# Optimization experiments

Hardware: AMD Instinct MI355X
Metric: run time of the kernel (lower is better)

## Reference

```python
import math
import jax, jax.numpy as jnp
import numpy as np

# Gemma4Audio config constants
HID = 1024
H = 8
D = HID // H            # 128
CHUNK = 12              # attention_chunk_size
PAST = 13 - 1           # max_past_horizon = context_left - 1
FUT = 0                 # max_future_horizon = context_right
CTX = CHUNK + PAST + FUT  # 24
SOFTCAP = 50.0
Q_SCALE = D ** (-0.5) / math.log(2)
K_SCALE = math.log(1.0 + math.e) / math.log(2)


def setup_inputs() -> dict:
    key = jax.random.key(0)
    ks = jax.random.split(key, 8)
    B, S = 4, 6144
    P = CTX + 1  # 25 relative positions
    std = HID ** (-0.5)
    return {
        "hidden_states": jax.random.normal(ks[0], (B, S, HID), jnp.float32),
        "position_embeddings": jax.random.normal(ks[1], (P, HID), jnp.float32),
        "Wq": jax.random.normal(ks[2], (HID, HID), jnp.float32) * std,
        "Wk": jax.random.normal(ks[3], (HID, HID), jnp.float32) * std,
        "Wv": jax.random.normal(ks[4], (HID, HID), jnp.float32) * std,
        "Wpost": jax.random.normal(ks[5], (HID, HID), jnp.float32) * std,
        "Wrel": jax.random.normal(ks[6], (HID, HID), jnp.float32) * std,
        "per_dim_scale": jnp.zeros((D,), jnp.float32),  # torch init: zeros
    }


def _extract_block_context(x, num_blocks):
    # x: [B, S, H, D] -> [B, num_blocks, CTX, H, D]
    xp = jnp.pad(x, ((0, 0), (PAST, FUT + CHUNK - 1), (0, 0), (0, 0)))
    idx = jnp.arange(num_blocks)[:, None] * CHUNK + jnp.arange(CTX)[None, :]
    return xp[:, idx]  # gather along seq axis


def _rel_shift(x):
    # x: [B, H, nb, CHUNK, P] -> [B, H, nb, CHUNK, CTX]
    B, Hh, nb, bs, pos_len = x.shape
    x = jnp.pad(x, ((0, 0), (0, 0), (0, 0), (0, 0), (0, CTX + 1 - pos_len)))
    x = x.reshape(B, Hh, nb, bs * (CTX + 1))[..., : bs * CTX]
    return x.reshape(B, Hh, nb, bs, CTX)


def reference(hidden_states, position_embeddings, Wq, Wk, Wv, Wpost, Wrel, per_dim_scale):
    B, S, _ = hidden_states.shape
    nb = (S + CHUNK - 1) // CHUNK
    pad = nb * CHUNK - S

    # Projections (ClippableLinear clamps are +/-inf at init -> identity)
    q = (hidden_states @ Wq.T).reshape(B, S, H, D)
    k = (hidden_states @ Wk.T).reshape(B, S, H, D)
    v = (hidden_states @ Wv.T).reshape(B, S, H, D)

    q = q * (Q_SCALE * jax.nn.softplus(per_dim_scale))  # per-dim scaled queries
    k = k * K_SCALE

    # [B, nb, CHUNK, H, D]
    q_blocked = jnp.pad(q, ((0, 0), (0, pad), (0, 0), (0, 0))).reshape(B, nb, CHUNK, H, D)
    k_ctx = _extract_block_context(k, nb)  # [B, nb, CTX, H, D]
    v_ctx = _extract_block_context(v, nb)

    # content score: [B, H, nb, CHUNK, CTX]
    matrix_ac = jnp.einsum('bnchd,bnkhd->bhnck', q_blocked, k_ctx)

    # relative position score
    rel_k = (position_embeddings @ Wrel.T).reshape(-1, H, D)  # [P, H, D]
    matrix_bd = jnp.einsum('bnchd,phd->bhncp', q_blocked, rel_k)
    matrix_bd = _rel_shift(matrix_bd)  # [B, H, nb, CHUNK, CTX]

    logits = matrix_ac + matrix_bd
    logits = jnp.tanh(logits / SOFTCAP) * SOFTCAP  # softcap
    attn = jax.nn.softmax(logits, axis=-1)

    out = jnp.einsum('bhnck,bnkhd->bnchd', attn, v_ctx)
    out = out.reshape(B, nb * CHUNK, H * D)[:, :S]
    return out @ Wpost.T
```

## Files before the change

kernel.cpp:

```cpp
#include <hip/hip_runtime.h>
#include <hip/hip_bf16.h>
#include <math.h>

typedef unsigned short ushort_t;
typedef __attribute__((ext_vector_type(8))) short short8;
typedef __attribute__((ext_vector_type(4))) short s4v;
typedef __attribute__((ext_vector_type(4))) float float4v;

#define HID 1024
#define NH 8
#define DH 128
#define CHUNK 12
#define PAST 12
#define CTX 24
#define NPOS 25
#define QKVW 3072

__device__ __forceinline__ float bf2f(ushort_t b){
  union{unsigned int u; float f;} x; x.u = ((unsigned int)b)<<16; return x.f;
}
__device__ __forceinline__ ushort_t f2bf(float f){
  union{float f; unsigned int u;} x; x.f = f;
  unsigned int u = x.u;
  unsigned int r = u + 0x7fffu + ((u>>16)&1u);
  return (ushort_t)(r>>16);
}

__device__ __forceinline__ void gload16(const ushort_t* g, ushort_t* l){
  __builtin_amdgcn_global_load_lds(
      (const __attribute__((address_space(1))) unsigned int*)g,
      (__attribute__((address_space(3))) unsigned int*)l,
      16, 0, 0);
}

__global__ __launch_bounds__(256) void cvt_f2b(
    const float* __restrict__ in, ushort_t* __restrict__ out, int n4)
{
  for (int i = blockIdx.x*256 + threadIdx.x; i < n4; i += gridDim.x*256){
    float4v v = ((const float4v*)in)[i];
    s4v o;
#pragma unroll
    for (int j=0;j<4;j++) o[j] = (short)f2bf(v[j]);
    ((s4v*)out)[i] = o;
  }
}

__global__ __launch_bounds__(256) void cvt_w4(
    const float* __restrict__ Wq, const float* __restrict__ Wk,
    const float* __restrict__ Wv, const float* __restrict__ Wp,
    ushort_t* __restrict__ Wcat, ushort_t* __restrict__ Wpb, int wsz4)
{
  for (int i = blockIdx.x*256 + threadIdx.x; i < 4*wsz4; i += gridDim.x*256){
    int seg = i / wsz4, off = i - seg*wsz4;
    const float* src = (seg==0) ? Wq : (seg==1) ? Wk : (seg==2) ? Wv : Wp;
    float4v v = ((const float4v*)src)[off];
    s4v o;
#pragma unroll
    for (int j=0;j<4;j++) o[j] = (short)f2bf(v[j]);
    if (seg < 3) ((s4v*)Wcat)[seg*wsz4 + off] = o;
    else         ((s4v*)Wpb)[off] = o;
  }
}

template<int MODE, int OUTF>
__global__ __launch_bounds__(512) void gemm8(
    const ushort_t* __restrict__ A, const ushort_t* __restrict__ W,
    void* __restrict__ Cv, int M, int N, int K,
    const float* __restrict__ pds, float qsc, float ksc)
{
  const int nwg  = gridDim.x;
  const int orig = blockIdx.x;
  const int qch  = nwg >> 3, rch = nwg & 7;
  const int xcd  = orig & 7, idx = orig >> 3;
  const int bid  = (xcd < rch ? xcd*(qch+1) : rch*(qch+1) + (xcd-rch)*qch) + idx;

  const int NT = N >> 8;
  const int m0 = (bid / NT) * 256;
  const int n0 = (bid % NT) * 256;

  const int tid  = threadIdx.x;
  const int w    = tid >> 6, lane = tid & 63;
  const int wm   = w >> 2, wn = w & 3;
  const int lr   = lane & 15;
  const int lg   = lane >> 4;

  __shared__ ushort_t lds[2][2][256*64];

  float4v acc[2][4][4];
#pragma unroll
  for (int mh=0; mh<2; mh++)
#pragma unroll
    for (int i=0;i<4;i++)
#pragma unroll
      for (int j=0;j<4;j++) acc[mh][i][j] = (float4v)0.0f;

  const int srow = lane >> 3;
  const int sg   = ((lane & 7) ^ srow) * 8;

  const ushort_t* Ab = A + (size_t)m0 * K;
  const ushort_t* Wb = W + (size_t)n0 * K;

#define STAGE_C(c, buf, kt) do {                                              \
    const int rr_ = (c)*64 + w*8 + srow;                                      \
    gload16(Ab + (size_t)rr_*K + (kt) + sg, &lds[buf][0][((c)*64 + w*8)*64]); \
    gload16(Wb + (size_t)rr_*K + (kt) + sg, &lds[buf][1][((c)*64 + w*8)*64]); \
  } while(0)

  short8 bfr[4];

#define PHASE(buf, mh, kh, LOADB) do {                                        \
    short8 afr[4];                                                            \
    _Pragma("unroll")                                                         \
    for (int i=0;i<4;i++){                                                    \
      const int r_ = wm*128 + (mh)*64 + i*16 + lr;                            \
      const int s_ = (((kh)>>3) + lg) ^ (r_ & 7);                             \
      afr[i] = *(const short8*)&lds[buf][0][r_*64 + s_*8];                    \
    }                                                                         \
    if (LOADB){                                                               \
      _Pragma("unroll")                                                       \
      for (int j=0;j<4;j++){                                                  \
        const int r_ = wn*64 + j*16 + lr;                                     \
        const int s_ = (((kh)>>3) + lg) ^ (r_ & 7);                           \
        bfr[j] = *(const short8*)&lds[buf][1][r_*64 + s_*8];                  \
      }                                                                       \
    }                                                                         \
    __builtin_amdgcn_s_setprio(1);                                            \
    _Pragma("unroll")                                                         \
    for (int i=0;i<4;i++)                                                     \
      _Pragma("unroll")                                                       \
      for (int j=0;j<4;j++)                                                   \
        acc[mh][i][j] = __builtin_amdgcn_mfma_f32_16x16x32_bf16(              \
            afr[i], bfr[j], acc[mh][i][j], 0,0,0);                            \
    __builtin_amdgcn_s_setprio(0);                                            \
    __builtin_amdgcn_s_barrier();                                             \
  } while(0)

  const int NTiles = K >> 6;
  STAGE_C(0, 0, 0); STAGE_C(1, 0, 0); STAGE_C(2, 0, 0); STAGE_C(3, 0, 0);
  __syncthreads();

  for (int t = 0; t < NTiles; ++t){
    const int cur = t & 1, nxt = cur ^ 1;
    const int ktn = (t+1) << 6;
    const bool pf = (t+1 < NTiles);
    if (pf) STAGE_C(0, nxt, ktn);
    PHASE(cur, 0, 0, 1);
    if (pf) STAGE_C(1, nxt, ktn);
    PHASE(cur, 1, 0, 0);
    if (pf) STAGE_C(2, nxt, ktn);
    PHASE(cur, 0, 32, 1);
    if (pf) STAGE_C(3, nxt, ktn);
    PHASE(cur, 1, 32, 0);
    __syncthreads();
  }
#undef STAGE_C
#undef PHASE

#pragma unroll
  for (int j=0;j<4;j++){
    const int col = n0 + wn*64 + j*16 + lr;
    float scale = 1.0f;
    if (MODE==1){
      if (col < 1024){ float p = pds[col & (DH-1)]; scale = qsc * log1pf(expf(p)); }
      else if (col < 2048) scale = ksc;
    }
#pragma unroll
    for (int mh=0; mh<2; mh++)
#pragma unroll
      for (int i=0;i<4;i++){
        const int row = m0 + wm*128 + mh*64 + i*16 + lg*4;
#pragma unroll
        for (int r=0;r<4;r++){
          float val = acc[mh][i][j][r] * scale;
          if (OUTF) ((float*)Cv)[(size_t)(row + r)*N + col] = val;
          else ((ushort_t*)Cv)[(size_t)(row + r)*N + col] = f2bf(val);
        }
      }
  }
}

template<int MODE, int OUTF>
__global__ __launch_bounds__(256) void gemm2(
    const ushort_t* __restrict__ A, const ushort_t* __restrict__ W,
    void* __restrict__ Cv, int M, int N, int K,
    const float* __restrict__ pds, float qsc, float ksc)
{
  const int nwg  = gridDim.x;
  const int orig = blockIdx.x;
  const int qch  = nwg >> 3, rch = nwg & 7;
  const int xcd  = orig & 7, idx = orig >> 3;
  const int bid  = (xcd < rch ? xcd*(qch+1) : rch*(qch+1) + (xcd-rch)*qch) + idx;

  const int NT = N >> 7;
  const int m0 = (bid / NT) * 128;
  const int n0 = (bid % NT) * 128;

  const int tid  = threadIdx.x;
  const int w    = tid >> 6, lane = tid & 63;
  const int wm   = w >> 1, wn = w & 1;
  const int lr   = lane & 15;
  const int lg   = lane >> 4;

  __shared__ ushort_t As0[128*32], Bs0[128*32];
  __shared__ ushort_t As1[128*32], Bs1[128*32];

  float4v acc[4][4];
#pragma unroll
  for (int i=0;i<4;i++)
#pragma unroll
    for (int j=0;j<4;j++) acc[i][j] = (float4v)0.0f;

  const int sr = lane >> 2;
  const int sc = (lane & 3) * 8;

  const ushort_t* Ab0 = A + (size_t)(m0 + w*16      + sr)*K + sc;
  const ushort_t* Ab1 = A + (size_t)(m0 + 64 + w*16 + sr)*K + sc;
  const ushort_t* Bb0 = W + (size_t)(n0 + w*16      + sr)*K + sc;
  const ushort_t* Bb1 = W + (size_t)(n0 + 64 + w*16 + sr)*K + sc;

#define STAGE(Abuf, Bbuf, kt) do {                    \
    gload16(Ab0 + (kt), &(Abuf)[(w*16)*32]);          \
    gload16(Ab1 + (kt), &(Abuf)[(64 + w*16)*32]);     \
    gload16(Bb0 + (kt), &(Bbuf)[(w*16)*32]);          \
    gload16(Bb1 + (kt), &(Bbuf)[(64 + w*16)*32]);     \
  } while(0)

#define COMPUTE(Abuf, Bbuf) do {                                             \
    short8 afr[4], bfr[4];                                                   \
    _Pragma("unroll")                                                        \
    for (int i=0;i<4;i++) afr[i] = *(const short8*)&(Abuf)[(wm*64 + i*16 + lr)*32 + lg*8]; \
    _Pragma("unroll")                                                        \
    for (int j=0;j<4;j++) bfr[j] = *(const short8*)&(Bbuf)[(wn*64 + j*16 + lr)*32 + lg*8]; \
    _Pragma("unroll")                                                        \
    for (int i=0;i<4;i++)                                                    \
      _Pragma("unroll")                                                      \
      for (int j=0;j<4;j++)                                                  \
        acc[i][j] = __builtin_amdgcn_mfma_f32_16x16x32_bf16(afr[i], bfr[j], acc[i][j], 0,0,0); \
  } while(0)

  const int nt = K >> 5;
  STAGE(As0, Bs0, 0);
  __syncthreads();

  for (int t = 0; t < nt; t += 2){
    if (t+1 < nt) STAGE(As1, Bs1, (t+1)*32);
    COMPUTE(As0, Bs0);
    __syncthreads();
    if (t+2 < nt) STAGE(As0, Bs0, (t+2)*32);
    COMPUTE(As1, Bs1);
    __syncthreads();
  }
#undef STAGE
#undef COMPUTE

#pragma unroll
  for (int j=0;j<4;j++){
    int col = n0 + wn*64 + j*16 + lr;
    float scale = 1.0f;
    if (MODE==1){
      if (col < 1024){ float p = pds[col & (DH-1)]; scale = qsc * log1pf(expf(p)); }
      else if (col < 2048) scale = ksc;
    }
#pragma unroll
    for (int i=0;i<4;i++){
      int row = m0 + wm*64 + i*16 + lg*4;
#pragma unroll
      for (int r=0;r<4;r++){
        float val = acc[i][j][r] * scale;
        if (OUTF) ((float*)Cv)[(size_t)(row + r)*N + col] = val;
        else ((ushort_t*)Cv)[(size_t)(row + r)*N + col] = f2bf(val);
      }
    }
  }
}

__global__ __launch_bounds__(256) void relk_kernel(
    const float* __restrict__ pe, const float* __restrict__ Wrel,
    ushort_t* __restrict__ rel)
{
  int gid = blockIdx.x*256 + threadIdx.x;
  if (gid >= NPOS*HID) return;
  int p = gid >> 10, n = gid & 1023;
  const float* a = pe + p*HID;
  const float* w = Wrel + (size_t)n*HID;
  float s = 0.f;
  for (int k=0;k<HID;k+=4){
    float4v av = *(const float4v*)(a+k);
    float4v wv = *(const float4v*)(w+k);
#pragma unroll
    for (int u=0;u<4;u++) s += av[u]*wv[u];
  }
  rel[gid] = f2bf(s);
}

__global__ __launch_bounds__(256) void attn_kernel(
  const ushort_t* __restrict__ qkv, const ushort_t* __restrict__ rel,
  ushort_t* __restrict__ o, int S)
{
  const int n0 = blockIdx.x * 4;
  const int b  = blockIdx.y, h = blockIdx.z;
  const int tid = threadIdx.x;
  const size_t bS = (size_t)b * S;

  __shared__ ushort_t ks[68][136];
  __shared__ ushort_t vt[128][68];
  __shared__ ushort_t rs[32][136];
  __shared__ float    sA[4][12][36];
  __shared__ float    sB[4][12][36];
  __shared__ ushort_t Pp[4][16][40];

  const int base = n0*CHUNK - PAST;
  {
    const int r0 = tid >> 4;
    const int c0 = (tid & 15) * 8;
    for (int r = r0; r < 68; r += 16){
      int s = base + r;
      short8 kv = (short8)0, vv = (short8)0;
      if (r < 60 && s >= 0 && s < S){
        kv = *(const short8*)&qkv[(bS + s)*QKVW + 1024 + h*DH + c0];
        vv = *(const short8*)&qkv[(bS + s)*QKVW + 2048 + h*DH + c0];
      }
      *(short8*)&ks[r][c0] = kv;
#pragma unroll
      for (int u=0;u<8;u++) vt[c0+u][r] = (ushort_t)vv[u];
    }
    for (int r = r0; r < 32; r += 16){
      short8 rv = (short8)0;
      if (r < NPOS) rv = *(const short8*)&rel[r*HID + h*DH + c0];
      *(short8*)&rs[r][c0] = rv;
    }
  }
  __syncthreads();

  const int w    = tid >> 6;
  const int lane = tid & 63;
  const int lr   = lane & 15;
  const int lg   = lane >> 4;

  int qrow = (n0 + w)*CHUNK + lr;
  if (qrow >= S) qrow = S - 1;
  const ushort_t* qp = qkv + (bS + qrow)*QKVW + h*DH + lg*8;
  short8 qf[4];
#pragma unroll
  for (int ks2=0; ks2<4; ks2++) qf[ks2] = *(const short8*)(qp + ks2*32);

#pragma unroll
  for (int t0=0; t0<2; t0++){
    float4v acc = (float4v)0.0f;
#pragma unroll
    for (int ks2=0; ks2<4; ks2++){
      short8 kf = *(const short8*)&ks[w*CHUNK + t0*16 + lr][ks2*32 + lg*8];
      acc = __builtin_amdgcn_mfma_f32_16x16x32_bf16(qf[ks2], kf, acc, 0,0,0);
    }
#pragma unroll
    for (int reg=0; reg<4; reg++){
      int cr = lg*4 + reg;
      if (cr < CHUNK) sA[w][cr][t0*16 + lr] = acc[reg];
    }
  }

#pragma unroll
  for (int t0=0; t0<2; t0++){
    float4v acc = (float4v)0.0f;
#pragma unroll
    for (int ks2=0; ks2<4; ks2++){
      short8 rf = *(const short8*)&rs[t0*16 + lr][ks2*32 + lg*8];
      acc = __builtin_amdgcn_mfma_f32_16x16x32_bf16(qf[ks2], rf, acc, 0,0,0);
    }
#pragma unroll
    for (int reg=0; reg<4; reg++){
      int cr = lg*4 + reg;
      if (cr < CHUNK) sB[w][cr][t0*16 + lr] = acc[reg];
    }
  }

#pragma unroll
  for (int i=0;i<2;i++){
    int idx = i*64 + lane;
    *(s4v*)&Pp[w][idx>>3][(idx&7)*4] = (s4v)0;
  }

  {
    const int c2 = lane >> 5;
    const int t  = lane & 31;
#pragma unroll
    for (int i=0;i<6;i++){
      int c = i*2 + c2;
      float x = -1e30f;
      if (t < CTX){
        int f = c*CTX + t;
        int r = f / NPOS, p = f - r*NPOS;
        x = sA[w][c][t] + sB[w][r][p];
        x = 50.0f * tanhf(x * 0.02f);
      }
      float m = x;
      for (int off=16; off>=1; off>>=1) m = fmaxf(m, __shfl_xor(m, off, 32));
      float e = (t < CTX) ? expf(x - m) : 0.0f;
      float s = e;
      for (int off=16; off>=1; off>>=1) s += __shfl_xor(s, off, 32);
      if (t < CTX) Pp[w][c][t] = f2bf(e / s);
    }
  }

  short8 pf = *(const short8*)&Pp[w][lr][lg*8];
  const int orow_base = (n0 + w)*CHUNK;
#pragma unroll
  for (int j=0; j<8; j++){
    int d  = j*16 + lr;
    int tb = w*CHUNK + lg*8;
    s4v b0 = *(const s4v*)&vt[d][tb];
    s4v b1 = *(const s4v*)&vt[d][tb+4];
    short8 bf;
#pragma unroll
    for (int u=0;u<4;u++){ bf[u] = b0[u]; bf[u+4] = b1[u]; }
    float4v a = __builtin_amdgcn_mfma_f32_16x16x32_bf16(pf, bf, (float4v)0.0f, 0,0,0);
#pragma unroll
    for (int reg=0; reg<4; reg++){
      int cr = lg*4 + reg;
      if (cr < CHUNK)
        o[(bS + orow_base + cr)*HID + h*DH + j*16 + lr] = f2bf(a[reg]);
    }
  }
}

extern "C" void kernel_launch(void* const* d_in, const int* in_sizes, int n_in,
                              void* d_out, int out_size, void* d_ws, size_t ws_size,
                              hipStream_t stream)
{
  const float* hs    = (const float*)d_in[0];
  const float* pe    = (const float*)d_in[1];
  const float* Wq    = (const float*)d_in[2];
  const float* Wk    = (const float*)d_in[3];
  const float* Wv    = (const float*)d_in[4];
  const float* Wpost = (const float*)d_in[5];
  const float* Wrel  = (const float*)d_in[6];
  const float* pds   = (const float*)d_in[7];
  float* out = (float*)d_out;

  const int BS = in_sizes[0] / HID;
  const int B  = 4;
  const int S  = BS / B;
  const int nb = S / CHUNK;

  const size_t per = (size_t)BS * HID;
  const size_t wsz = (size_t)HID * HID;
  ushort_t* qkv  = (ushort_t*)d_ws;
  ushort_t* at   = qkv  + (size_t)BS * QKVW;
  ushort_t* rel  = at   + per;
  ushort_t* hsb  = rel  + (size_t)NPOS*HID;
  ushort_t* Wcat = hsb  + per;
  ushort_t* Wpb  = Wcat + 3*wsz;

  const float qsc = (float)(pow((double)DH, -0.5) / log(2.0));
  const float ksc = (float)(log(1.0 + exp(1.0)) / log(2.0));

  cvt_f2b<<<2048, 256, 0, stream>>>(hs, hsb, (int)(per/4));
  cvt_w4<<<2048, 256, 0, stream>>>(Wq, Wk, Wv, Wpost, Wcat, Wpb, (int)(wsz/4));

  gemm8<1,0><<<(BS/256)*(QKVW/256), 512, 0, stream>>>(
      hsb, Wcat, qkv, BS, QKVW, HID, pds, qsc, ksc);
  relk_kernel<<<(NPOS*HID + 255)/256, 256, 0, stream>>>(pe, Wrel, rel);
  attn_kernel<<<dim3(nb/4, B, NH), 256, 0, stream>>>(qkv, rel, at, S);
  gemm2<0,1><<<(BS/128)*(HID/128), 256, 0, stream>>>(
      at, Wpb, out, BS, HID, HID, nullptr, 1.0f, 1.0f);
}
```

Baseline: 441.1 us.

## Rework QKV GEMM into a 4-stage K=32 LDS pipeline with vmcnt waits

```diff
diff --git a/kernel.cpp b/kernel.cpp
--- a/kernel.cpp
+++ b/kernel.cpp
@@ -63,7 +63,7 @@
 }
 
 template<int MODE, int OUTF>
-__global__ __launch_bounds__(512) void gemm8(
+__global__ __launch_bounds__(512, 2) void gemm8v2(
     const ushort_t* __restrict__ A, const ushort_t* __restrict__ W,
     void* __restrict__ Cv, int M, int N, int K,
     const float* __restrict__ pds, float qsc, float ksc)
@@ -83,78 +83,62 @@
   const int wm   = w >> 2, wn = w & 3;
   const int lr   = lane & 15;
   const int lg   = lane >> 4;
-
-  __shared__ ushort_t lds[2][2][256*64];
-
-  float4v acc[2][4][4];
-#pragma unroll
-  for (int mh=0; mh<2; mh++)
-#pragma unroll
-    for (int i=0;i<4;i++)
-#pragma unroll
-      for (int j=0;j<4;j++) acc[mh][i][j] = (float4v)0.0f;
-
-  const int srow = lane >> 3;
-  const int sg   = ((lane & 7) ^ srow) * 8;
-
-  const ushort_t* Ab = A + (size_t)m0 * K;
-  const ushort_t* Wb = W + (size_t)n0 * K;
-
-#define STAGE_C(c, buf, kt) do {                                              \
-    const int rr_ = (c)*64 + w*8 + srow;                                      \
-    gload16(Ab + (size_t)rr_*K + (kt) + sg, &lds[buf][0][((c)*64 + w*8)*64]); \
-    gload16(Wb + (size_t)rr_*K + (kt) + sg, &lds[buf][1][((c)*64 + w*8)*64]); \
+  const int kswz = (lg ^ (lr & 3)) * 8;
+
+  __shared__ ushort_t lds[4][2][256*32];
+
+  float4v acc[8][4];
+#pragma unroll
+  for (int i=0;i<8;i++)
+#pragma unroll
+    for (int j=0;j<4;j++) acc[i][j] = (float4v)0.0f;
+
+  const int rowin = lane >> 2;
+  const int kg    = ((lane & 3) ^ (rowin & 3)) * 8;
+  const ushort_t* A0 = A + (size_t)(m0 + w*16 + rowin)*K + kg;
+  const ushort_t* A1 = A0 + (size_t)128*K;
+  const ushort_t* B0 = W + (size_t)(n0 + w*16 + rowin)*K + kg;
+  const ushort_t* B1 = B0 + (size_t)128*K;
+
+#define STAGEP(slot, ko) do {                              \
+    gload16(A0 + (ko), &lds[slot][0][(w*16)*32]);          \
+    gload16(A1 + (ko), &lds[slot][0][(128 + w*16)*32]);    \
+    gload16(B0 + (ko), &lds[slot][1][(w*16)*32]);          \
+    gload16(B1 + (ko), &lds[slot][1][(128 + w*16)*32]);    \
   } while(0)
 
-  short8 bfr[4];
-
-#define PHASE(buf, mh, kh, LOADB) do {                                        \
-    short8 afr[4];                                                            \
-    _Pragma("unroll")                                                         \
-    for (int i=0;i<4;i++){                                                    \
-      const int r_ = wm*128 + (mh)*64 + i*16 + lr;                            \
-      const int s_ = (((kh)>>3) + lg) ^ (r_ & 7);                             \
-      afr[i] = *(const short8*)&lds[buf][0][r_*64 + s_*8];                    \
-    }                                                                         \
-    if (LOADB){                                                               \
-      _Pragma("unroll")                                                       \
-      for (int j=0;j<4;j++){                                                  \
-        const int r_ = wn*64 + j*16 + lr;                                     \
-        const int s_ = (((kh)>>3) + lg) ^ (r_ & 7);                           \
-        bfr[j] = *(const short8*)&lds[buf][1][r_*64 + s_*8];                  \
-      }                                                                       \
-    }                                                                         \
-    __builtin_amdgcn_s_setprio(1);                                            \
-    _Pragma("unroll")                                                         \
-    for (int i=0;i<4;i++)                                                     \
-      _Pragma("unroll")                                                       \
-      for (int j=0;j<4;j++)                                                   \
-        acc[mh][i][j] = __builtin_amdgcn_mfma_f32_16x16x32_bf16(              \
-            afr[i], bfr[j], acc[mh][i][j], 0,0,0);                            \
-    __builtin_amdgcn_s_setprio(0);                                            \
-    __builtin_amdgcn_s_barrier();                                             \
+#define PH(i, DOSTAGE, VM) do {                                              \
+    asm volatile("s_waitcnt vmcnt(" #VM ")" ::: "memory");                   \
+    __builtin_amdgcn_s_barrier();                                            \
+    __builtin_amdgcn_sched_barrier(0);                                       \
+    if (DOSTAGE){ STAGEP((((i)+3)&3), kn); kn += 32; }                       \
+    short8 bfr[4];                                                           \
+    _Pragma("unroll")                                                        \
+    for (int j=0;j<4;j++)                                                    \
+      bfr[j] = *(const short8*)&lds[i][1][(wn*64 + j*16 + lr)*32 + kswz];    \
+    __builtin_amdgcn_s_setprio(1);                                           \
+    _Pragma("unroll")                                                        \
+    for (int ii=0; ii<8; ii++){                                              \
+      short8 afr = *(const short8*)&lds[i][0][(wm*128 + ii*16 + lr)*32 + kswz]; \
+      _Pragma("unroll")                                                      \
+      for (int j=0;j<4;j++)                                                  \
+        acc[ii][j] = __builtin_amdgcn_mfma_f32_16x16x32_bf16(                \
+            afr, bfr[j], acc[ii][j], 0,0,0);                                 \
+    }                                                                        \
+    __builtin_amdgcn_s_setprio(0);                                           \
+    __builtin_amdgcn_sched_barrier(0);                                       \
   } while(0)
 
-  const int NTiles = K >> 6;
-  STAGE_C(0, 0, 0); STAGE_C(1, 0, 0); STAGE_C(2, 0, 0); STAGE_C(3, 0, 0);
-  __syncthreads();
-
-  for (int t = 0; t < NTiles; ++t){
-    const int cur = t & 1, nxt = cur ^ 1;
-    const int ktn = (t+1) << 6;
-    const bool pf = (t+1 < NTiles);
-    if (pf) STAGE_C(0, nxt, ktn);
-    PHASE(cur, 0, 0, 1);
-    if (pf) STAGE_C(1, nxt, ktn);
-    PHASE(cur, 1, 0, 0);
-    if (pf) STAGE_C(2, nxt, ktn);
-    PHASE(cur, 0, 32, 1);
-    if (pf) STAGE_C(3, nxt, ktn);
-    PHASE(cur, 1, 32, 0);
-    __syncthreads();
-  }
-#undef STAGE_C
-#undef PHASE
+  const int T = K >> 5;
+  STAGEP(0, 0); STAGEP(1, 32); STAGEP(2, 64);
+  int kn = 96;
+
+  for (int pb = 0; pb <= T - 8; pb += 4){
+    PH(0,1,8); PH(1,1,8); PH(2,1,8); PH(3,1,8);
+  }
+  PH(0,1,8); PH(1,0,8); PH(2,0,4); PH(3,0,0);
+#undef STAGEP
+#undef PH
 
 #pragma unroll
   for (int j=0;j<4;j++){
@@ -165,17 +149,15 @@
       else if (col < 2048) scale = ksc;
     }
 #pragma unroll
-    for (int mh=0; mh<2; mh++)
-#pragma unroll
-      for (int i=0;i<4;i++){
-        const int row = m0 + wm*128 + mh*64 + i*16 + lg*4;
-#pragma unroll
-        for (int r=0;r<4;r++){
-          float val = acc[mh][i][j][r] * scale;
-          if (OUTF) ((float*)Cv)[(size_t)(row + r)*N + col] = val;
-          else ((ushort_t*)Cv)[(size_t)(row + r)*N + col] = f2bf(val);
-        }
+    for (int i=0;i<8;i++){
+      const int row = m0 + wm*128 + i*16 + lg*4;
+#pragma unroll
+      for (int r=0;r<4;r++){
+        float val = acc[i][j][r] * scale;
+        if (OUTF) ((float*)Cv)[(size_t)(row + r)*N + col] = val;
+        else ((ushort_t*)Cv)[(size_t)(row + r)*N + col] = f2bf(val);
       }
+    }
   }
 }
 
@@ -457,7 +439,7 @@
   cvt_f2b<<<2048, 256, 0, stream>>>(hs, hsb, (int)(per/4));
   cvt_w4<<<2048, 256, 0, stream>>>(Wq, Wk, Wv, Wpost, Wcat, Wpb, (int)(wsz/4));
 
-  gemm8<1,0><<<(BS/256)*(QKVW/256), 512, 0, stream>>>(
+  gemm8v2<1,0><<<(BS/256)*(QKVW/256), 512, 0, stream>>>(
       hsb, Wcat, qkv, BS, QKVW, HID, pds, qsc, ksc);
   relk_kernel<<<(NPOS*HID + 255)/256, 256, 0, stream>>>(pe, Wrel, rel);
   attn_kernel<<<dim3(nb/4, B, NH), 256, 0, stream>>>(qkv, rel, at, S);
```

Result: no change. 440.1 us (-0.2%).
